# Kernel tuning notes

Measured on AMD Instinct MI355X. Metric: run time of the kernel, lower is better.

Reference implementation:

```python
import jax, jax.numpy as jnp
import numpy as np

N, E, G = 100000, 400000, 2000
F_IN, HID, H = 74, 64, 4
HID4 = HID * H           # 256, per-node feature after flatten(1)
POOL = 3 * HID4          # 768, concat(mean, max, sum)
OUT = 128
NEG_SLOPE = 0.2          # DGL GATConv default LeakyReLU slope


def setup_inputs() -> dict:
    key = jax.random.key(0)
    ks = jax.random.split(key, 20)
    p = lambda k, shape: (jax.random.normal(k, shape, jnp.float32) * 0.05)
    inp = {
        "node_feat": jax.random.normal(ks[0], (N, F_IN), jnp.float32),
        "src": jax.random.randint(ks[1], (E,), 0, N, jnp.int32),
        "dst": jax.random.randint(ks[2], (E,), 0, N, jnp.int32),
        # every graph gets exactly N//G nodes (sorted, non-empty segments)
        "graph_ids": jnp.arange(N, dtype=jnp.int32) // (N // G),
        "enc_W": p(ks[3], (F_IN, HID)), "enc_b": jnp.zeros((HID,), jnp.float32),
    }
    in_dims = [HID, HID4, HID4]
    for l in range(3):
        inp[f"W{l}"] = p(ks[4 + 4 * l], (in_dims[l], H * HID))
        inp[f"al{l}"] = p(ks[5 + 4 * l], (H, HID))
        inp[f"ar{l}"] = p(ks[6 + 4 * l], (H, HID))
        inp[f"b{l}"] = jnp.zeros((H * HID,), jnp.float32)
    inp["r1_W"] = p(ks[16], (POOL, HID)); inp["r1_b"] = jnp.zeros((HID,), jnp.float32)
    inp["r2_W"] = p(ks[17], (HID, OUT)); inp["r2_b"] = jnp.zeros((OUT,), jnp.float32)
    return inp


def _gat_layer(h, src, dst, W, al, ar, b):
    # DGL GATConv (eval mode: dropouts are identity), activation=ReLU
    z = (h @ W).reshape(N, H, HID)                       # [N,H,O]
    el = jnp.einsum("nho,ho->nh", z, al)                 # [N,H]
    er = jnp.einsum("nho,ho->nh", z, ar)
    e = jax.nn.leaky_relu(el[src] + er[dst], NEG_SLOPE)  # [E,H]
    # segment softmax over incoming edges of each dst node, per head
    m = jax.ops.segment_max(e, dst, num_segments=N)      # [N,H]
    ex = jnp.exp(e - m[dst])
    s = jax.ops.segment_sum(ex, dst, num_segments=N)     # [N,H]
    a = ex / s[dst]                                      # [E,H]
    out = jax.ops.segment_sum(z[src] * a[:, :, None], dst, num_segments=N)
    out = out + b.reshape(1, H, HID)                     # GATConv bias
    return jax.nn.relu(out).reshape(N, HID4)             # flatten(1)


def reference(node_feat, src, dst, graph_ids, enc_W, enc_b,
              W0, al0, ar0, b0, W1, al1, ar1, b1, W2, al2, ar2, b2,
              r1_W, r1_b, r2_W, r2_b):
    h = node_feat @ enc_W + enc_b                        # node encoder
    h = _gat_layer(h, src, dst, W0, al0, ar0, b0)
    h = _gat_layer(h, src, dst, W1, al1, ar1, b1)
    h = _gat_layer(h, src, dst, W2, al2, ar2, b2)
    # multi-pool readout: mean / max / sum over nodes of each graph
    h_sum = jax.ops.segment_sum(h, graph_ids, num_segments=G)
    cnt = jax.ops.segment_sum(jnp.ones((N, 1), h.dtype), graph_ids, num_segments=G)
    h_mean = h_sum / cnt
    h_max = jax.ops.segment_max(h, graph_ids, num_segments=G)
    hg = jnp.concatenate([h_mean, h_max, h_sum], axis=1)  # [G, 3*HID4]
    hg = jax.nn.relu(hg @ r1_W + r1_b)
    return hg @ r2_W + r2_b                              # [G, OUT]
```

## Files before the change

### kernel.cpp

```cpp
#include <hip/hip_runtime.h>

#define N_NODES 100000
#define N_EDGES 400000
#define N_GRAPHS 2000
#define F_IN 74
#define ENC_KP 96
#define HID 64
#define NHEAD 4
#define HID4 256
#define OUT_DIM 128
#define NODES_PER_G 50

typedef __attribute__((ext_vector_type(8))) short short8;
typedef __attribute__((ext_vector_type(4))) float f32x4;

__device__ inline ushort f2bf(float f) {
  union { float f; unsigned u; } v; v.f = f;
  unsigned u = v.u;
  return (ushort)((u + 0x7FFFu + ((u >> 16) & 1u)) >> 16);
}
__device__ inline float bf2f(ushort b) {
  union { unsigned u; float f; } v; v.u = ((unsigned)b) << 16;
  return v.f;
}
__device__ inline float leaky(float x) { return x >= 0.f ? x : 0.2f * x; }

__device__ inline void glds16(const ushort* g, ushort* l) {
  __builtin_amdgcn_global_load_lds(
      (const __attribute__((address_space(1))) void*)g,
      (__attribute__((address_space(3))) void*)l, 16, 0, 0);
}

__global__ __launch_bounds__(256) void k_count(const int* __restrict__ dst,
                                               int* __restrict__ off) {
  int e = blockIdx.x * 256 + threadIdx.x;
  if (e < N_EDGES) atomicAdd(&off[dst[e] + 1], 1);
}

__global__ __launch_bounds__(256) void k_scan1(int* __restrict__ data, int n,
                                               int* __restrict__ blksum) {
  __shared__ int sh[256];
  int t = threadIdx.x;
  int base = blockIdx.x * 1024 + t * 4;
  int v0 = (base + 0 < n) ? data[base + 0] : 0;
  int v1 = (base + 1 < n) ? data[base + 1] : 0;
  int v2 = (base + 2 < n) ? data[base + 2] : 0;
  int v3 = (base + 3 < n) ? data[base + 3] : 0;
  v1 += v0; v2 += v1; v3 += v2;
  int tot = v3;
  sh[t] = tot;
  __syncthreads();
  for (int o = 1; o < 256; o <<= 1) {
    int x = (t >= o) ? sh[t - o] : 0;
    __syncthreads();
    sh[t] += x;
    __syncthreads();
  }
  int excl = sh[t] - tot;
  if (base + 0 < n) data[base + 0] = v0 + excl;
  if (base + 1 < n) data[base + 1] = v1 + excl;
  if (base + 2 < n) data[base + 2] = v2 + excl;
  if (base + 3 < n) data[base + 3] = v3 + excl;
  if (t == 255) blksum[blockIdx.x] = sh[255];
}

__global__ __launch_bounds__(256) void k_scan2(int* __restrict__ blksum, int nb) {
  __shared__ int sh[256];
  int t = threadIdx.x;
  sh[t] = (t < nb) ? blksum[t] : 0;
  __syncthreads();
  for (int o = 1; o < 256; o <<= 1) {
    int x = (t >= o) ? sh[t - o] : 0;
    __syncthreads();
    sh[t] += x;
    __syncthreads();
  }
  if (t < nb) blksum[t] = sh[t];
}

__global__ __launch_bounds__(256) void k_scan3(int* __restrict__ data, int n,
                                               const int* __restrict__ blksum) {
  int b = blockIdx.x;
  if (b == 0) return;
  int add = blksum[b - 1];
  int base = b * 1024 + threadIdx.x * 4;
  for (int j = 0; j < 4; ++j)
    if (base + j < n) data[base + j] += add;
}

__global__ __launch_bounds__(256) void k_scatter(const int* __restrict__ dst,
                                                 const int* __restrict__ src,
                                                 const int* __restrict__ off,
                                                 int* __restrict__ cursor,
                                                 int* __restrict__ srcs) {
  int e = blockIdx.x * 256 + threadIdx.x;
  if (e >= N_EDGES) return;
  int d = dst[e];
  int pos = off[d] + atomicAdd(&cursor[d], 1);
  srcs[pos] = src[e];
}

__global__ __launch_bounds__(256) void k_sortseg(const int* __restrict__ off,
                                                 int* __restrict__ srcs) {
  int n = blockIdx.x * 256 + threadIdx.x;
  if (n >= N_NODES) return;
  int beg = off[n], end = off[n + 1];
  for (int i = beg + 1; i < end; ++i) {
    int key = srcs[i];
    int j = i - 1;
    while (j >= beg && srcs[j] > key) { srcs[j + 1] = srcs[j]; --j; }
    srcs[j + 1] = key;
  }
}

__global__ __launch_bounds__(256) void k_prep(
    const float* __restrict__ enc_W,
    const float* __restrict__ W0, const float* __restrict__ W1,
    const float* __restrict__ W2,
    const float* __restrict__ al0, const float* __restrict__ ar0,
    const float* __restrict__ al1, const float* __restrict__ ar1,
    const float* __restrict__ al2, const float* __restrict__ ar2,
    ushort* __restrict__ Wte,
    ushort* __restrict__ Wt0, ushort* __restrict__ Wt1,
    ushort* __restrict__ Wt2,
    ushort* __restrict__ Wlr0, ushort* __restrict__ Wlr1,
    ushort* __restrict__ Wlr2) {
  const int S0 = HID * ENC_KP;
  const int S1 = S0 + HID * HID4;
  const int S2 = S1 + HID4 * HID4;
  const int S3 = S2 + HID4 * HID4;
  const int S4 = S3 + 16 * HID;
  const int S5 = S4 + 16 * HID4;
  const int S6 = S5 + 16 * HID4;
  int idx = blockIdx.x * 256 + threadIdx.x;
  if (idx < S0) {
    int col = idx / ENC_KP, k = idx - col * ENC_KP;
    Wte[idx] = (k < F_IN) ? f2bf(enc_W[(size_t)k * HID + col]) : (ushort)0;
  } else if (idx < S1) {
    int i = idx - S0; int k = i >> 8, n = i & 255;
    Wt0[(size_t)n * HID + k] = f2bf(W0[i]);
  } else if (idx < S2) {
    int i = idx - S1; int k = i >> 8, n = i & 255;
    Wt1[(size_t)n * HID4 + k] = f2bf(W1[i]);
  } else if (idx < S3) {
    int i = idx - S2; int k = i >> 8, n = i & 255;
    Wt2[(size_t)n * HID4 + k] = f2bf(W2[i]);
  } else if (idx < S4) {
    int i = idx - S3; int c = i / HID, k = i - c * HID;
    float acc = 0.f;
    if (c < 8) {
      const float* av = (c < 4) ? al0 + (c & 3) * 64 : ar0 + (c & 3) * 64;
      const float* wp = W0 + (size_t)k * HID4 + (c & 3) * 64;
      for (int o = 0; o < 64; ++o) acc = fmaf(wp[o], av[o], acc);
    }
    Wlr0[(size_t)c * HID + k] = f2bf(acc);
  } else if (idx < S5) {
    int i = idx - S4; int c = i / HID4, k = i - c * HID4;
    float acc = 0.f;
    if (c < 8) {
      const float* av = (c < 4) ? al1 + (c & 3) * 64 : ar1 + (c & 3) * 64;
      const float* wp = W1 + (size_t)k * HID4 + (c & 3) * 64;
      for (int o = 0; o < 64; ++o) acc = fmaf(wp[o], av[o], acc);
    }
    Wlr1[(size_t)c * HID4 + k] = f2bf(acc);
  } else if (idx < S6) {
    int i = idx - S5; int c = i / HID4, k = i - c * HID4;
    float acc = 0.f;
    if (c < 8) {
      const float* av = (c < 4) ? al2 + (c & 3) * 64 : ar2 + (c & 3) * 64;
      const float* wp = W2 + (size_t)k * HID4 + (c & 3) * 64;
      for (int o = 0; o < 64; ++o) acc = fmaf(wp[o], av[o], acc);
    }
    Wlr2[(size_t)c * HID4 + k] = f2bf(acc);
  }
}

__global__ __launch_bounds__(256) void k_enc_mfma(const float* __restrict__ nf,
                                                  const ushort* __restrict__ Bt,
                                                  const float* __restrict__ bias,
                                                  ushort* __restrict__ Cb) {
  __shared__ ushort As[128][104];
  __shared__ ushort Bs[64][104];
  int t = threadIdx.x;
  int lane = t & 63;
  int wid = t >> 6;
  int brow = blockIdx.x * 128;

  for (int i = t; i < 128 * ENC_KP; i += 256) {
    int r = i / ENC_KP;
    int c = i - r * ENC_KP;
    int gr = brow + r;
    float v = 0.f;
    if (gr < N_NODES && c < F_IN) v = nf[(size_t)gr * F_IN + c];
    As[r][c] = f2bf(v);
  }
  if (t < 128) {
    int r = t >> 1;
    int o = (t & 1) * 48;
#pragma unroll
    for (int i = 0; i < 6; ++i)
      *(int4*)&Bs[r][o + i * 8] = *(const int4*)(Bt + (size_t)r * ENC_KP + o + i * 8);
  }
  __syncthreads();

  int fr = lane & 15;
  int ko = (lane >> 4) * 8;
  f32x4 acc[2][4];
#pragma unroll
  for (int m = 0; m < 2; ++m)
#pragma unroll
    for (int n = 0; n < 4; ++n) acc[m][n] = (f32x4)(0.f);

#pragma unroll
  for (int ks = 0; ks < 3; ++ks) {
    short8 a[2], b[4];
#pragma unroll
    for (int m = 0; m < 2; ++m) a[m] = *(const short8*)&As[wid * 32 + m * 16 + fr][ks * 32 + ko];
#pragma unroll
    for (int n = 0; n < 4; ++n) b[n] = *(const short8*)&Bs[n * 16 + fr][ks * 32 + ko];
#pragma unroll
    for (int m = 0; m < 2; ++m)
#pragma unroll
      for (int n = 0; n < 4; ++n)
        acc[m][n] = __builtin_amdgcn_mfma_f32_16x16x32_bf16(a[m], b[n], acc[m][n], 0, 0, 0);
  }

  int r0 = (lane >> 4) * 4;
  int cc = lane & 15;
#pragma unroll
  for (int m = 0; m < 2; ++m) {
#pragma unroll
    for (int j = 0; j < 4; ++j) {
      int row = brow + wid * 32 + m * 16 + r0 + j;
      if (row >= N_NODES) continue;
#pragma unroll
      for (int n = 0; n < 4; ++n) {
        int col = n * 16 + cc;
        Cb[(size_t)row * HID + col] = f2bf(acc[m][n][j] + bias[col]);
      }
    }
  }
}

template <int K>
__global__ __launch_bounds__(256) void k_gemm_mfma(const ushort* __restrict__ A,
                                                   const ushort* __restrict__ Bt,
                                                   const ushort* __restrict__ Wlr,
                                                   ushort* __restrict__ Cb,
                                                   float* __restrict__ el,
                                                   float* __restrict__ er,
                                                   int n_rows) {
  __shared__ __align__(16) ushort As[2][128 * 32];
  __shared__ __align__(16) ushort Bs[2][128 * 32];
  int bid = blockIdx.x;
  int rpan = (bid >> 4) * 8 + (bid & 7);
  int nrp = (n_rows + 127) / 128;
  if (rpan >= nrp) return;
  int brow = rpan * 128;
  int bcol = ((bid >> 3) & 1) * 128;

  int t = threadIdx.x;
  int lane = t & 63;
  int wid = t >> 6;
  int wr = wid >> 1, wc = wid & 1;

  f32x4 acc[4][4];
#pragma unroll
  for (int m = 0; m < 4; ++m)
#pragma unroll
    for (int n = 0; n < 4; ++n) acc[m][n] = (f32x4)(0.f);

  int srow0 = (wid * 2 + 0) * 16 + (lane >> 2);
  int srow1 = (wid * 2 + 1) * 16 + (lane >> 2);
  int skc = (lane & 3) * 8;
  int ga0 = brow + srow0; if (ga0 > n_rows - 1) ga0 = n_rows - 1;
  int ga1 = brow + srow1; if (ga1 > n_rows - 1) ga1 = n_rows - 1;
  const ushort* pa0 = A + (size_t)ga0 * K + skc;
  const ushort* pa1 = A + (size_t)ga1 * K + skc;
  const ushort* pb0 = Bt + (size_t)(bcol + srow0) * K + skc;
  const ushort* pb1 = Bt + (size_t)(bcol + srow1) * K + skc;
  int lo0 = (wid * 2 + 0) * 512;
  int lo1 = (wid * 2 + 1) * 512;

  int fr = lane & 15;
  int ko = (lane >> 4) * 8;

  bool do_lr = (bcol == 0) && (wc == 0);
  short8 blrr[K / 32];
  f32x4 acc_lr[4];
#pragma unroll
  for (int m = 0; m < 4; ++m) acc_lr[m] = (f32x4)(0.f);
  if (do_lr) {
#pragma unroll
    for (int ks = 0; ks < K / 32; ++ks)
      blrr[ks] = *(const short8*)(Wlr + (size_t)fr * K + ks * 32 + ko);
  }

  glds16(pa0, &As[0][lo0]);
  glds16(pa1, &As[0][lo1]);
  glds16(pb0, &Bs[0][lo0]);
  glds16(pb1, &Bs[0][lo1]);
  __syncthreads();

#pragma unroll
  for (int kstep = 0; kstep < K / 32; ++kstep) {
    int k0 = kstep * 32;
    int cur = kstep & 1;
    if (k0 + 32 < K) {
      glds16(pa0 + k0 + 32, &As[cur ^ 1][lo0]);
      glds16(pa1 + k0 + 32, &As[cur ^ 1][lo1]);
      glds16(pb0 + k0 + 32, &Bs[cur ^ 1][lo0]);
      glds16(pb1 + k0 + 32, &Bs[cur ^ 1][lo1]);
    }
    short8 a[4], b[4];
#pragma unroll
    for (int m = 0; m < 4; ++m)
      a[m] = *(const short8*)(&As[cur][0] + (wr * 64 + m * 16 + fr) * 32 + ko);
#pragma unroll
    for (int n = 0; n < 4; ++n)
      b[n] = *(const short8*)(&Bs[cur][0] + (wc * 64 + n * 16 + fr) * 32 + ko);
#pragma unroll
    for (int m = 0; m < 4; ++m)
#pragma unroll
      for (int n = 0; n < 4; ++n)
        acc[m][n] = __builtin_amdgcn_mfma_f32_16x16x32_bf16(a[m], b[n], acc[m][n], 0, 0, 0);
    if (do_lr) {
#pragma unroll
      for (int m = 0; m < 4; ++m)
        acc_lr[m] = __builtin_amdgcn_mfma_f32_16x16x32_bf16(a[m], blrr[kstep], acc_lr[m], 0, 0, 0);
    }
    __syncthreads();
  }

  int r0 = (lane >> 4) * 4;
  int cc = lane & 15;
#pragma unroll
  for (int m = 0; m < 4; ++m) {
#pragma unroll
    for (int j = 0; j < 4; ++j) {
      int row = brow + wr * 64 + m * 16 + r0 + j;
      if (row >= n_rows) continue;
#pragma unroll
      for (int n = 0; n < 4; ++n)
        Cb[(size_t)row * HID4 + bcol + wc * 64 + n * 16 + cc] = f2bf(acc[m][n][j]);
    }
  }
  if (do_lr && cc < 8) {
#pragma unroll
    for (int m = 0; m < 4; ++m)
#pragma unroll
      for (int j = 0; j < 4; ++j) {
        int row = brow + wr * 64 + m * 16 + r0 + j;
        if (row >= n_rows) continue;
        float v = acc_lr[m][j];
        if (cc < 4) el[(size_t)row * NHEAD + cc] = v;
        else er[(size_t)row * NHEAD + (cc - 4)] = v;
      }
  }
}

__global__ __launch_bounds__(256) void k_agg(const ushort* __restrict__ zb,
                                             const float* __restrict__ el,
                                             const float* __restrict__ er,
                                             const int* __restrict__ off,
                                             const int* __restrict__ srcs,
                                             const float* __restrict__ bias,
                                             ushort* __restrict__ outb) {
  int w = (blockIdx.x * 256 + threadIdx.x) >> 6;
  int lane = threadIdx.x & 63;
  int n = w * 4 + (lane >> 4);
  int li = lane & 15;
  if (n >= N_NODES) return;
  int h = li >> 2;
  int c = li * 16;
  int beg = off[n], end = off[n + 1];
  float erh = er[(size_t)n * NHEAD + h];

  float s = 0.f;
  float acc[16];
#pragma unroll
  for (int j = 0; j < 16; ++j) acc[j] = 0.f;

  float e0 = 0.f, e1 = 0.f, e2 = 0.f;
  int4 za0 = make_int4(0, 0, 0, 0), zb0 = za0;
  int4 za1 = za0, zb1 = za0, za2 = za0, zb2 = za0;
  if (beg < end) {
    int sn = srcs[beg];
    e0 = el[(size_t)sn * NHEAD + h];
    const ushort* zp = zb + (size_t)sn * HID4 + c;
    za0 = *(const int4*)zp; zb0 = *(const int4*)(zp + 8);
  }
  if (beg + 1 < end) {
    int sn = srcs[beg + 1];
    e1 = el[(size_t)sn * NHEAD + h];
    const ushort* zp = zb + (size_t)sn * HID4 + c;
    za1 = *(const int4*)zp; zb1 = *(const int4*)(zp + 8);
  }
  if (beg + 2 < end) {
    int sn = srcs[beg + 2];
    e2 = el[(size_t)sn * NHEAD + h];
    const ushort* zp = zb + (size_t)sn * HID4 + c;
    za2 = *(const int4*)zp; zb2 = *(const int4*)(zp + 8);
  }

  for (int p = beg; p < end; ++p) {
    float ev = e0;
    int4 va = za0, vb = zb0;
    e0 = e1; za0 = za1; zb0 = zb1;
    e1 = e2; za1 = za2; zb1 = zb2;
    if (p + 3 < end) {
      int sn = srcs[p + 3];
      e2 = el[(size_t)sn * NHEAD + h];
      const ushort* zp = zb + (size_t)sn * HID4 + c;
      za2 = *(const int4*)zp; zb2 = *(const int4*)(zp + 8);
    }
    float pv = __expf(leaky(ev + erh));
    s += pv;
    const ushort* ua = (const ushort*)&va;
    const ushort* ub = (const ushort*)&vb;
#pragma unroll
    for (int j = 0; j < 8; ++j) acc[j] = fmaf(pv, bf2f(ua[j]), acc[j]);
#pragma unroll
    for (int j = 0; j < 8; ++j) acc[8 + j] = fmaf(pv, bf2f(ub[j]), acc[8 + j]);
  }
  float inv = (s > 0.f) ? 1.f / s : 0.f;
  float bb[16];
#pragma unroll
  for (int j = 0; j < 16; j += 4) {
    float4 b4 = *(const float4*)(bias + c + j);
    bb[j] = b4.x; bb[j + 1] = b4.y; bb[j + 2] = b4.z; bb[j + 3] = b4.w;
  }
  int4 ov0, ov1;
  ushort* os0 = (ushort*)&ov0;
  ushort* os1 = (ushort*)&ov1;
#pragma unroll
  for (int j = 0; j < 8; ++j) os0[j] = f2bf(fmaxf(acc[j] * inv + bb[j], 0.f));
#pragma unroll
  for (int j = 0; j < 8; ++j) os1[j] = f2bf(fmaxf(acc[8 + j] * inv + bb[8 + j], 0.f));
  ushort* op = outb + (size_t)n * HID4 + c;
  *(int4*)op = ov0;
  *(int4*)(op + 8) = ov1;
}

__global__ __launch_bounds__(256) void k_pool_mlp(const ushort* __restrict__ h,
                                                  const float* __restrict__ r1W,
                                                  const float* __restrict__ r1b,
                                                  const float* __restrict__ r2W,
                                                  const float* __restrict__ r2b,
                                                  float* __restrict__ out) {
  __shared__ float pooled[3 * HID4];
  __shared__ float part[4][HID];
  __shared__ float mid[HID];
  int g = blockIdx.x;
  int t = threadIdx.x;
  const ushort* base = h + (size_t)g * NODES_PER_G * HID4;
  float sum = 0.f, mx = -1e30f;
  for (int i = 0; i < NODES_PER_G; ++i) {
    float v = bf2f(base[(size_t)i * HID4 + t]);
    sum += v;
    mx = fmaxf(mx, v);
  }
  pooled[t] = sum / (float)NODES_PER_G;
  pooled[HID4 + t] = mx;
  pooled[2 * HID4 + t] = sum;
  __syncthreads();
  {
    int o = t & 63, chunk = t >> 6;
    float acc = 0.f;
    int k0 = chunk * 192;
    for (int k = k0; k < k0 + 192; ++k) acc = fmaf(pooled[k], r1W[k * HID + o], acc);
    part[chunk][o] = acc;
  }
  __syncthreads();
  if (t < HID) {
    float acc = r1b[t] + part[0][t] + part[1][t] + part[2][t] + part[3][t];
    mid[t] = fmaxf(acc, 0.f);
  }
  __syncthreads();
  if (t < OUT_DIM) {
    float acc = r2b[t];
    for (int k = 0; k < HID; ++k) acc = fmaf(mid[k], r2W[k * OUT_DIM + t], acc);
    out[(size_t)g * OUT_DIM + t] = acc;
  }
}

extern "C" void kernel_launch(void* const* d_in, const int* in_sizes, int n_in,
                              void* d_out, int out_size, void* d_ws, size_t ws_size,
                              hipStream_t stream) {
  const float* node_feat = (const float*)d_in[0];
  const int* src = (const int*)d_in[1];
  const int* dst = (const int*)d_in[2];
  const float* enc_W = (const float*)d_in[4];
  const float* enc_b = (const float*)d_in[5];
  const float* Wl[3] = {(const float*)d_in[6], (const float*)d_in[10], (const float*)d_in[14]};
  const float* all_[3] = {(const float*)d_in[7], (const float*)d_in[11], (const float*)d_in[15]};
  const float* arl[3] = {(const float*)d_in[8], (const float*)d_in[12], (const float*)d_in[16]};
  const float* bl[3] = {(const float*)d_in[9], (const float*)d_in[13], (const float*)d_in[17]};
  const float* r1W = (const float*)d_in[18];
  const float* r1b = (const float*)d_in[19];
  const float* r2W = (const float*)d_in[20];
  const float* r2b = (const float*)d_in[21];
  float* out = (float*)d_out;

  char* p = (char*)d_ws;
  auto alloc = [&](size_t bytes) {
    void* r = (void*)p;
    p += (bytes + 255) & ~(size_t)255;
    return r;
  };
  int* off = (int*)alloc((N_NODES + 1) * sizeof(int));
  int* cursor = (int*)alloc(N_NODES * sizeof(int));
  int* srcs = (int*)alloc(N_EDGES * sizeof(int));
  int* blksum = (int*)alloc(256 * sizeof(int));
  float* el = (float*)alloc((size_t)N_NODES * NHEAD * sizeof(float));
  float* er = (float*)alloc((size_t)N_NODES * NHEAD * sizeof(float));
  ushort* Qb = (ushort*)alloc((size_t)N_NODES * HID4 * sizeof(ushort));
  ushort* Pb = (ushort*)alloc((size_t)N_NODES * HID4 * sizeof(ushort));
  ushort* Wte = (ushort*)alloc((size_t)HID * ENC_KP * sizeof(ushort));
  ushort* Wt0 = (ushort*)alloc((size_t)HID4 * HID * sizeof(ushort));
  ushort* Wt1 = (ushort*)alloc((size_t)HID4 * HID4 * sizeof(ushort));
  ushort* Wt2 = (ushort*)alloc((size_t)HID4 * HID4 * sizeof(ushort));
  ushort* Wlr0 = (ushort*)alloc((size_t)16 * HID * sizeof(ushort));
  ushort* Wlr1 = (ushort*)alloc((size_t)16 * HID4 * sizeof(ushort));
  ushort* Wlr2 = (ushort*)alloc((size_t)16 * HID4 * sizeof(ushort));

  hipMemsetAsync(off, 0, (N_NODES + 1) * sizeof(int), stream);
  hipMemsetAsync(cursor, 0, N_NODES * sizeof(int), stream);
  k_count<<<(N_EDGES + 255) / 256, 256, 0, stream>>>(dst, off);
  const int SCAN_N = N_NODES + 1;
  const int NB = (SCAN_N + 1023) / 1024;
  k_scan1<<<NB, 256, 0, stream>>>(off, SCAN_N, blksum);
  k_scan2<<<1, 256, 0, stream>>>(blksum, NB);
  k_scan3<<<NB, 256, 0, stream>>>(off, SCAN_N, blksum);
  k_scatter<<<(N_EDGES + 255) / 256, 256, 0, stream>>>(dst, src, off, cursor, srcs);
  k_sortseg<<<(N_NODES + 255) / 256, 256, 0, stream>>>(off, srcs);

  const int PREP_N = HID * ENC_KP + HID * HID4 + 2 * HID4 * HID4 +
                     16 * (HID + HID4 + HID4);
  k_prep<<<(PREP_N + 255) / 256, 256, 0, stream>>>(
      enc_W, Wl[0], Wl[1], Wl[2], all_[0], arl[0], all_[1], arl[1], all_[2], arl[2],
      Wte, Wt0, Wt1, Wt2, Wlr0, Wlr1, Wlr2);

  k_enc_mfma<<<(N_NODES + 127) / 128, 256, 0, stream>>>(node_feat, Wte, enc_b, Pb);

  const int NRP = (N_NODES + 127) / 128;
  const int GEMM_BLOCKS = ((NRP + 7) / 8) * 16;
  const int AGG_BLOCKS = ((N_NODES + 3) / 4 + 3) / 4;
  const ushort* Wts[3] = {Wt0, Wt1, Wt2};
  const ushort* Wlrs[3] = {Wlr0, Wlr1, Wlr2};
  for (int l = 0; l < 3; ++l) {
    if (l == 0)
      k_gemm_mfma<HID><<<GEMM_BLOCKS, 256, 0, stream>>>(Pb, Wts[0], Wlrs[0], Qb, el, er, N_NODES);
    else
      k_gemm_mfma<HID4><<<GEMM_BLOCKS, 256, 0, stream>>>(Pb, Wts[l], Wlrs[l], Qb, el, er, N_NODES);
    k_agg<<<AGG_BLOCKS, 256, 0, stream>>>(Qb, el, er, off, srcs, bl[l], Pb);
  }

  k_pool_mlp<<<N_GRAPHS, 256, 0, stream>>>(Pb, r1W, r1b, r2W, r2b, out);
}
```

Before: 355.9 us.

## Fold node encoder into layer-0 GAT projection via precomposed weights

```diff
diff --git a/kernel.cpp b/kernel.cpp
--- a/kernel.cpp
+++ b/kernel.cpp
@@ -114,77 +114,107 @@
 }
 
 __global__ __launch_bounds__(256) void k_prep(
-    const float* __restrict__ enc_W,
+    const float* __restrict__ enc_W, const float* __restrict__ enc_b,
     const float* __restrict__ W0, const float* __restrict__ W1,
     const float* __restrict__ W2,
     const float* __restrict__ al0, const float* __restrict__ ar0,
     const float* __restrict__ al1, const float* __restrict__ ar1,
     const float* __restrict__ al2, const float* __restrict__ ar2,
-    ushort* __restrict__ Wte,
-    ushort* __restrict__ Wt0, ushort* __restrict__ Wt1,
-    ushort* __restrict__ Wt2,
-    ushort* __restrict__ Wlr0, ushort* __restrict__ Wlr1,
-    ushort* __restrict__ Wlr2) {
-  const int S0 = HID * ENC_KP;
-  const int S1 = S0 + HID * HID4;
-  const int S2 = S1 + HID4 * HID4;
-  const int S3 = S2 + HID4 * HID4;
-  const int S4 = S3 + 16 * HID;
-  const int S5 = S4 + 16 * HID4;
+    ushort* __restrict__ Wcomb, float* __restrict__ bcomb,
+    ushort* __restrict__ Wlrc, float* __restrict__ elc,
+    ushort* __restrict__ Wt1, ushort* __restrict__ Wt2,
+    ushort* __restrict__ Wlr1, ushort* __restrict__ Wlr2) {
+  const int S0 = HID4 * ENC_KP;
+  const int S1 = S0 + HID4;
+  const int S2 = S1 + 16 * ENC_KP;
+  const int S3 = S2 + 8;
+  const int S4 = S3 + HID4 * HID4;
+  const int S5 = S4 + HID4 * HID4;
   const int S6 = S5 + 16 * HID4;
+  const int S7 = S6 + 16 * HID4;
   int idx = blockIdx.x * 256 + threadIdx.x;
   if (idx < S0) {
-    int col = idx / ENC_KP, k = idx - col * ENC_KP;
-    Wte[idx] = (k < F_IN) ? f2bf(enc_W[(size_t)k * HID + col]) : (ushort)0;
+    int c = idx / ENC_KP, k = idx - c * ENC_KP;
+    float acc = 0.f;
+    if (k < F_IN) {
+      const float* we = enc_W + (size_t)k * HID;
+      for (int o = 0; o < HID; ++o) acc = fmaf(we[o], W0[(size_t)o * HID4 + c], acc);
+    }
+    Wcomb[idx] = f2bf(acc);
   } else if (idx < S1) {
-    int i = idx - S0; int k = i >> 8, n = i & 255;
-    Wt0[(size_t)n * HID + k] = f2bf(W0[i]);
+    int c = idx - S0;
+    float acc = 0.f;
+    for (int o = 0; o < HID; ++o) acc = fmaf(enc_b[o], W0[(size_t)o * HID4 + c], acc);
+    bcomb[c] = acc;
   } else if (idx < S2) {
-    int i = idx - S1; int k = i >> 8, n = i & 255;
+    int i = idx - S1;
+    int c = i / ENC_KP, k = i - c * ENC_KP;
+    float acc = 0.f;
+    if (c < 8 && k < F_IN) {
+      const float* av = (c < 4) ? al0 + (c & 3) * 64 : ar0 + (c & 3) * 64;
+      const float* we = enc_W + (size_t)k * HID;
+      for (int o = 0; o < HID; ++o) {
+        float w = 0.f;
+        const float* wp = W0 + (size_t)o * HID4 + (c & 3) * 64;
+        for (int j = 0; j < 64; ++j) w = fmaf(wp[j], av[j], w);
+        acc = fmaf(we[o], w, acc);
+      }
+    }
+    Wlrc[i] = f2bf(acc);
+  } else if (idx < S3) {
+    int c = idx - S2;
+    float acc = 0.f;
+    const float* av = (c < 4) ? al0 + (c & 3) * 64 : ar0 + (c & 3) * 64;
+    for (int o = 0; o < HID; ++o) {
+      float w = 0.f;
+      const float* wp = W0 + (size_t)o * HID4 + (c & 3) * 64;
+      for (int j = 0; j < 64; ++j) w = fmaf(wp[j], av[j], w);
+      acc = fmaf(enc_b[o], w, acc);
+    }
+    elc[c] = acc;
+  } else if (idx < S4) {
+    int i = idx - S3; int k = i >> 8, n = i & 255;
     Wt1[(size_t)n * HID4 + k] = f2bf(W1[i]);
-  } else if (idx < S3) {
-    int i = idx - S2; int k = i >> 8, n = i & 255;
+  } else if (idx < S5) {
+    int i = idx - S4; int k = i >> 8, n = i & 255;
     Wt2[(size_t)n * HID4 + k] = f2bf(W2[i]);
-  } else if (idx < S4) {
-    int i = idx - S3; int c = i / HID, k = i - c * HID;
-    float acc = 0.f;
-    if (c < 8) {
-      const float* av = (c < 4) ? al0 + (c & 3) * 64 : ar0 + (c & 3) * 64;
-      const float* wp = W0 + (size_t)k * HID4 + (c & 3) * 64;
-      for (int o = 0; o < 64; ++o) acc = fmaf(wp[o], av[o], acc);
-    }
-    Wlr0[(size_t)c * HID + k] = f2bf(acc);
-  } else if (idx < S5) {
-    int i = idx - S4; int c = i / HID4, k = i - c * HID4;
+  } else if (idx < S6) {
+    int i = idx - S5; int c = i / HID4, k = i - c * HID4;
     float acc = 0.f;
     if (c < 8) {
       const float* av = (c < 4) ? al1 + (c & 3) * 64 : ar1 + (c & 3) * 64;
       const float* wp = W1 + (size_t)k * HID4 + (c & 3) * 64;
       for (int o = 0; o < 64; ++o) acc = fmaf(wp[o], av[o], acc);
     }
-    Wlr1[(size_t)c * HID4 + k] = f2bf(acc);
-  } else if (idx < S6) {
-    int i = idx - S5; int c = i / HID4, k = i - c * HID4;
+    Wlr1[i] = f2bf(acc);
+  } else if (idx < S7) {
+    int i = idx - S6; int c = i / HID4, k = i - c * HID4;
     float acc = 0.f;
     if (c < 8) {
       const float* av = (c < 4) ? al2 + (c & 3) * 64 : ar2 + (c & 3) * 64;
       const float* wp = W2 + (size_t)k * HID4 + (c & 3) * 64;
       for (int o = 0; o < 64; ++o) acc = fmaf(wp[o], av[o], acc);
     }
-    Wlr2[(size_t)c * HID4 + k] = f2bf(acc);
-  }
-}
-
-__global__ __launch_bounds__(256) void k_enc_mfma(const float* __restrict__ nf,
-                                                  const ushort* __restrict__ Bt,
-                                                  const float* __restrict__ bias,
-                                                  ushort* __restrict__ Cb) {
+    Wlr2[i] = f2bf(acc);
+  }
+}
+
+__global__ __launch_bounds__(256) void k_gemm0(const float* __restrict__ nf,
+                                               const ushort* __restrict__ Bt,
+                                               const ushort* __restrict__ Wlr,
+                                               const float* __restrict__ bcomb,
+                                               const float* __restrict__ elc,
+                                               ushort* __restrict__ Cb,
+                                               float* __restrict__ el,
+                                               float* __restrict__ er) {
   __shared__ ushort As[128][104];
-  __shared__ ushort Bs[64][104];
+  __shared__ ushort Bs[128][104];
   int t = threadIdx.x;
   int lane = t & 63;
   int wid = t >> 6;
+  int wr = wid >> 1, wc = wid & 1;
   int brow = blockIdx.x * 128;
+  int bcol = blockIdx.y * 128;
 
   for (int i = t; i < 128 * ENC_KP; i += 256) {
     int r = i / ENC_KP;
@@ -194,51 +224,78 @@
     if (gr < N_NODES && c < F_IN) v = nf[(size_t)gr * F_IN + c];
     As[r][c] = f2bf(v);
   }
-  if (t < 128) {
+  {
     int r = t >> 1;
     int o = (t & 1) * 48;
 #pragma unroll
     for (int i = 0; i < 6; ++i)
-      *(int4*)&Bs[r][o + i * 8] = *(const int4*)(Bt + (size_t)r * ENC_KP + o + i * 8);
+      *(int4*)&Bs[r][o + i * 8] =
+          *(const int4*)(Bt + (size_t)(bcol + r) * ENC_KP + o + i * 8);
   }
   __syncthreads();
 
   int fr = lane & 15;
   int ko = (lane >> 4) * 8;
-  f32x4 acc[2][4];
-#pragma unroll
-  for (int m = 0; m < 2; ++m)
+  bool do_lr = (bcol == 0) && (wc == 0);
+
+  f32x4 acc[4][4];
+#pragma unroll
+  for (int m = 0; m < 4; ++m)
 #pragma unroll
     for (int n = 0; n < 4; ++n) acc[m][n] = (f32x4)(0.f);
+  f32x4 acc_lr[4];
+#pragma unroll
+  for (int m = 0; m < 4; ++m) acc_lr[m] = (f32x4)(0.f);
 
 #pragma unroll
   for (int ks = 0; ks < 3; ++ks) {
-    short8 a[2], b[4];
-#pragma unroll
-    for (int m = 0; m < 2; ++m) a[m] = *(const short8*)&As[wid * 32 + m * 16 + fr][ks * 32 + ko];
-#pragma unroll
-    for (int n = 0; n < 4; ++n) b[n] = *(const short8*)&Bs[n * 16 + fr][ks * 32 + ko];
-#pragma unroll
-    for (int m = 0; m < 2; ++m)
+    short8 a[4], b[4];
+#pragma unroll
+    for (int m = 0; m < 4; ++m)
+      a[m] = *(const short8*)&As[wr * 64 + m * 16 + fr][ks * 32 + ko];
+#pragma unroll
+    for (int n = 0; n < 4; ++n)
+      b[n] = *(const short8*)&Bs[wc * 64 + n * 16 + fr][ks * 32 + ko];
+#pragma unroll
+    for (int m = 0; m < 4; ++m)
 #pragma unroll
       for (int n = 0; n < 4; ++n)
         acc[m][n] = __builtin_amdgcn_mfma_f32_16x16x32_bf16(a[m], b[n], acc[m][n], 0, 0, 0);
+    if (do_lr) {
+      short8 blr = *(const short8*)(Wlr + (size_t)fr * ENC_KP + ks * 32 + ko);
+#pragma unroll
+      for (int m = 0; m < 4; ++m)
+        acc_lr[m] = __builtin_amdgcn_mfma_f32_16x16x32_bf16(a[m], blr, acc_lr[m], 0, 0, 0);
+    }
   }
 
   int r0 = (lane >> 4) * 4;
   int cc = lane & 15;
 #pragma unroll
-  for (int m = 0; m < 2; ++m) {
+  for (int m = 0; m < 4; ++m) {
 #pragma unroll
     for (int j = 0; j < 4; ++j) {
-      int row = brow + wid * 32 + m * 16 + r0 + j;
+      int row = brow + wr * 64 + m * 16 + r0 + j;
       if (row >= N_NODES) continue;
 #pragma unroll
       for (int n = 0; n < 4; ++n) {
-        int col = n * 16 + cc;
-        Cb[(size_t)row * HID + col] = f2bf(acc[m][n][j] + bias[col]);
+        int col = bcol + wc * 64 + n * 16 + cc;
+        Cb[(size_t)row * HID4 + col] = f2bf(acc[m][n][j] + bcomb[col]);
       }
     }
+  }
+  if (do_lr && cc < 8) {
+    float ec = elc[cc];
+#pragma unroll
+    for (int m = 0; m < 4; ++m)
+#pragma unroll
+      for (int j = 0; j < 4; ++j) {
+        int row = brow + wr * 64 + m * 16 + r0 + j;
+        if (row >= N_NODES) continue;
+        float v = acc_lr[m][j] + ec;
+        if (cc < 4) el[(size_t)row * NHEAD + cc] = v;
+        else er[(size_t)row * NHEAD + (cc - 4)] = v;
+      }
   }
 }
 
@@ -516,11 +573,12 @@
   float* er = (float*)alloc((size_t)N_NODES * NHEAD * sizeof(float));
   ushort* Qb = (ushort*)alloc((size_t)N_NODES * HID4 * sizeof(ushort));
   ushort* Pb = (ushort*)alloc((size_t)N_NODES * HID4 * sizeof(ushort));
-  ushort* Wte = (ushort*)alloc((size_t)HID * ENC_KP * sizeof(ushort));
-  ushort* Wt0 = (ushort*)alloc((size_t)HID4 * HID * sizeof(ushort));
+  ushort* Wcomb = (ushort*)alloc((size_t)HID4 * ENC_KP * sizeof(ushort));
+  float* bcomb = (float*)alloc((size_t)HID4 * sizeof(float));
+  ushort* Wlrc = (ushort*)alloc((size_t)16 * ENC_KP * sizeof(ushort));
+  float* elc = (float*)alloc(8 * sizeof(float));
   ushort* Wt1 = (ushort*)alloc((size_t)HID4 * HID4 * sizeof(ushort));
   ushort* Wt2 = (ushort*)alloc((size_t)HID4 * HID4 * sizeof(ushort));
-  ushort* Wlr0 = (ushort*)alloc((size_t)16 * HID * sizeof(ushort));
   ushort* Wlr1 = (ushort*)alloc((size_t)16 * HID4 * sizeof(ushort));
   ushort* Wlr2 = (ushort*)alloc((size_t)16 * HID4 * sizeof(ushort));
 
@@ -535,25 +593,25 @@
   k_scatter<<<(N_EDGES + 255) / 256, 256, 0, stream>>>(dst, src, off, cursor, srcs);
   k_sortseg<<<(N_NODES + 255) / 256, 256, 0, stream>>>(off, srcs);
 
-  const int PREP_N = HID * ENC_KP + HID * HID4 + 2 * HID4 * HID4 +
-                     16 * (HID + HID4 + HID4);
+  const int PREP_N = HID4 * ENC_KP + HID4 + 16 * ENC_KP + 8 +
+                     2 * HID4 * HID4 + 2 * 16 * HID4;
   k_prep<<<(PREP_N + 255) / 256, 256, 0, stream>>>(
-      enc_W, Wl[0], Wl[1], Wl[2], all_[0], arl[0], all_[1], arl[1], all_[2], arl[2],
-      Wte, Wt0, Wt1, Wt2, Wlr0, Wlr1, Wlr2);
-
-  k_enc_mfma<<<(N_NODES + 127) / 128, 256, 0, stream>>>(node_feat, Wte, enc_b, Pb);
+      enc_W, enc_b, Wl[0], Wl[1], Wl[2],
+      all_[0], arl[0], all_[1], arl[1], all_[2], arl[2],
+      Wcomb, bcomb, Wlrc, elc, Wt1, Wt2, Wlr1, Wlr2);
 
   const int NRP = (N_NODES + 127) / 128;
+  const int AGG_BLOCKS = ((N_NODES + 3) / 4 + 3) / 4;
+  dim3 g0grid(NRP, 2);
+  k_gemm0<<<g0grid, 256, 0, stream>>>(node_feat, Wcomb, Wlrc, bcomb, elc, Qb, el, er);
+  k_agg<<<AGG_BLOCKS, 256, 0, stream>>>(Qb, el, er, off, srcs, bl[0], Pb);
+
   const int GEMM_BLOCKS = ((NRP + 7) / 8) * 16;
-  const int AGG_BLOCKS = ((N_NODES + 3) / 4 + 3) / 4;
-  const ushort* Wts[3] = {Wt0, Wt1, Wt2};
-  const ushort* Wlrs[3] = {Wlr0, Wlr1, Wlr2};
-  for (int l = 0; l < 3; ++l) {
-    if (l == 0)
-      k_gemm_mfma<HID><<<GEMM_BLOCKS, 256, 0, stream>>>(Pb, Wts[0], Wlrs[0], Qb, el, er, N_NODES);
-    else
-      k_gemm_mfma<HID4><<<GEMM_BLOCKS, 256, 0, stream>>>(Pb, Wts[l], Wlrs[l], Qb, el, er, N_NODES);
-    k_agg<<<AGG_BLOCKS, 256, 0, stream>>>(Qb, el, er, off, srcs, bl[l], Pb);
+  const ushort* Wts[2] = {Wt1, Wt2};
+  const ushort* Wlrs[2] = {Wlr1, Wlr2};
+  for (int l = 0; l < 2; ++l) {
+    k_gemm_mfma<HID4><<<GEMM_BLOCKS, 256, 0, stream>>>(Pb, Wts[l], Wlrs[l], Qb, el, er, N_NODES);
+    k_agg<<<AGG_BLOCKS, 256, 0, stream>>>(Qb, el, er, off, srcs, bl[l + 1], Pb);
   }
 
   k_pool_mlp<<<N_GRAPHS, 256, 0, stream>>>(Pb, r1W, r1b, r2W, r2b, out);
```

After: 462.2 us. 1.3x slower.

## Fuse last GAT layer aggregation with graph pooling and readout MLP

Applied to the files above, without the earlier changes.

```diff
diff --git a/kernel.cpp b/kernel.cpp
--- a/kernel.cpp
+++ b/kernel.cpp
@@ -442,28 +442,125 @@
   *(int4*)(op + 8) = ov1;
 }
 
-__global__ __launch_bounds__(256) void k_pool_mlp(const ushort* __restrict__ h,
-                                                  const float* __restrict__ r1W,
-                                                  const float* __restrict__ r1b,
-                                                  const float* __restrict__ r2W,
-                                                  const float* __restrict__ r2b,
-                                                  float* __restrict__ out) {
+__global__ __launch_bounds__(256) void k_agg_pool(
+    const ushort* __restrict__ zb, const float* __restrict__ el,
+    const float* __restrict__ er, const int* __restrict__ off,
+    const int* __restrict__ srcs, const float* __restrict__ bias,
+    const float* __restrict__ r1W, const float* __restrict__ r1b,
+    const float* __restrict__ r2W, const float* __restrict__ r2b,
+    float* __restrict__ out) {
+  __shared__ float sumb[4][HID4];
+  __shared__ float maxb[4][HID4];
   __shared__ float pooled[3 * HID4];
   __shared__ float part[4][HID];
   __shared__ float mid[HID];
   int g = blockIdx.x;
   int t = threadIdx.x;
-  const ushort* base = h + (size_t)g * NODES_PER_G * HID4;
-  float sum = 0.f, mx = -1e30f;
-  for (int i = 0; i < NODES_PER_G; ++i) {
-    float v = bf2f(base[(size_t)i * HID4 + t]);
-    sum += v;
-    mx = fmaxf(mx, v);
-  }
-  pooled[t] = sum / (float)NODES_PER_G;
-  pooled[HID4 + t] = mx;
-  pooled[2 * HID4 + t] = sum;
-  __syncthreads();
+  int w = t >> 6;
+  int lane = t & 63;
+  int grp = lane >> 4;
+  int li = lane & 15;
+  int h = li >> 2;
+  int c = li * 16;
+
+  float bb[16];
+#pragma unroll
+  for (int j = 0; j < 16; j += 4) {
+    float4 b4 = *(const float4*)(bias + c + j);
+    bb[j] = b4.x; bb[j + 1] = b4.y; bb[j + 2] = b4.z; bb[j + 3] = b4.w;
+  }
+
+  float psum[16], pmax[16];
+#pragma unroll
+  for (int j = 0; j < 16; ++j) { psum[j] = 0.f; pmax[j] = -1e30f; }
+
+  for (int it = 0; it < 4; ++it) {
+    int slot = it * 16 + w * 4 + grp;
+    if (slot < NODES_PER_G) {
+      int n = g * NODES_PER_G + slot;
+      int beg = off[n], end = off[n + 1];
+      float erh = er[(size_t)n * NHEAD + h];
+      float s = 0.f;
+      float acc[16];
+#pragma unroll
+      for (int j = 0; j < 16; ++j) acc[j] = 0.f;
+
+      float e0 = 0.f, e1 = 0.f, e2 = 0.f;
+      int4 za0 = make_int4(0, 0, 0, 0), zb0 = za0;
+      int4 za1 = za0, zb1 = za0, za2 = za0, zb2 = za0;
+      if (beg < end) {
+        int sn = srcs[beg];
+        e0 = el[(size_t)sn * NHEAD + h];
+        const ushort* zp = zb + (size_t)sn * HID4 + c;
+        za0 = *(const int4*)zp; zb0 = *(const int4*)(zp + 8);
+      }
+      if (beg + 1 < end) {
+        int sn = srcs[beg + 1];
+        e1 = el[(size_t)sn * NHEAD + h];
+        const ushort* zp = zb + (size_t)sn * HID4 + c;
+        za1 = *(const int4*)zp; zb1 = *(const int4*)(zp + 8);
+      }
+      if (beg + 2 < end) {
+        int sn = srcs[beg + 2];
+        e2 = el[(size_t)sn * NHEAD + h];
+        const ushort* zp = zb + (size_t)sn * HID4 + c;
+        za2 = *(const int4*)zp; zb2 = *(const int4*)(zp + 8);
+      }
+      for (int p = beg; p < end; ++p) {
+        float ev = e0;
+        int4 va = za0, vb = zb0;
+        e0 = e1; za0 = za1; zb0 = zb1;
+        e1 = e2; za1 = za2; zb1 = zb2;
+        if (p + 3 < end) {
+          int sn = srcs[p + 3];
+          e2 = el[(size_t)sn * NHEAD + h];
+          const ushort* zp = zb + (size_t)sn * HID4 + c;
+          za2 = *(const int4*)zp; zb2 = *(const int4*)(zp + 8);
+        }
+        float pv = __expf(leaky(ev + erh));
+        s += pv;
+        const ushort* ua = (const ushort*)&va;
+        const ushort* ub = (const ushort*)&vb;
+#pragma unroll
+        for (int j = 0; j < 8; ++j) acc[j] = fmaf(pv, bf2f(ua[j]), acc[j]);
+#pragma unroll
+        for (int j = 0; j < 8; ++j) acc[8 + j] = fmaf(pv, bf2f(ub[j]), acc[8 + j]);
+      }
+      float inv = (s > 0.f) ? 1.f / s : 0.f;
+#pragma unroll
+      for (int j = 0; j < 16; ++j) {
+        float v = bf2f(f2bf(fmaxf(acc[j] * inv + bb[j], 0.f)));
+        psum[j] += v;
+        pmax[j] = fmaxf(pmax[j], v);
+      }
+    }
+  }
+
+#pragma unroll
+  for (int j = 0; j < 16; ++j) {
+    psum[j] += __shfl_xor(psum[j], 16, 64);
+    psum[j] += __shfl_xor(psum[j], 32, 64);
+    pmax[j] = fmaxf(pmax[j], __shfl_xor(pmax[j], 16, 64));
+    pmax[j] = fmaxf(pmax[j], __shfl_xor(pmax[j], 32, 64));
+  }
+  if (lane < 16) {
+#pragma unroll
+    for (int j = 0; j < 16; ++j) {
+      sumb[w][c + j] = psum[j];
+      maxb[w][c + j] = pmax[j];
+    }
+  }
+  __syncthreads();
+
+  {
+    float ssum = sumb[0][t] + sumb[1][t] + sumb[2][t] + sumb[3][t];
+    float smax = fmaxf(fmaxf(maxb[0][t], maxb[1][t]), fmaxf(maxb[2][t], maxb[3][t]));
+    pooled[t] = ssum / (float)NODES_PER_G;
+    pooled[HID4 + t] = smax;
+    pooled[2 * HID4 + t] = ssum;
+  }
+  __syncthreads();
+
   {
     int o = t & 63, chunk = t >> 6;
     float acc = 0.f;
@@ -546,15 +643,12 @@
   const int NRP = (N_NODES + 127) / 128;
   const int GEMM_BLOCKS = ((NRP + 7) / 8) * 16;
   const int AGG_BLOCKS = ((N_NODES + 3) / 4 + 3) / 4;
-  const ushort* Wts[3] = {Wt0, Wt1, Wt2};
-  const ushort* Wlrs[3] = {Wlr0, Wlr1, Wlr2};
-  for (int l = 0; l < 3; ++l) {
-    if (l == 0)
-      k_gemm_mfma<HID><<<GEMM_BLOCKS, 256, 0, stream>>>(Pb, Wts[0], Wlrs[0], Qb, el, er, N_NODES);
-    else
-      k_gemm_mfma<HID4><<<GEMM_BLOCKS, 256, 0, stream>>>(Pb, Wts[l], Wlrs[l], Qb, el, er, N_NODES);
-    k_agg<<<AGG_BLOCKS, 256, 0, stream>>>(Qb, el, er, off, srcs, bl[l], Pb);
-  }
-
-  k_pool_mlp<<<N_GRAPHS, 256, 0, stream>>>(Pb, r1W, r1b, r2W, r2b, out);
-}
+  k_gemm_mfma<HID><<<GEMM_BLOCKS, 256, 0, stream>>>(Pb, Wt0, Wlr0, Qb, el, er, N_NODES);
+  k_agg<<<AGG_BLOCKS, 256, 0, stream>>>(Qb, el, er, off, srcs, bl[0], Pb);
+  k_gemm_mfma<HID4><<<GEMM_BLOCKS, 256, 0, stream>>>(Pb, Wt1, Wlr1, Qb, el, er, N_NODES);
+  k_agg<<<AGG_BLOCKS, 256, 0, stream>>>(Qb, el, er, off, srcs, bl[1], Pb);
+
+  k_gemm_mfma<HID4><<<GEMM_BLOCKS, 256, 0, stream>>>(Pb, Wt2, Wlr2, Qb, el, er, N_NODES);
+  k_agg_pool<<<N_GRAPHS, 256, 0, stream>>>(Qb, el, er, off, srcs, bl[2],
+                                           r1W, r1b, r2W, r2b, out);
+}
```

Measured after the change: 352.8 us. About the same (-0.9%).
